# Optimization experiments

Measured on AMD Instinct MI355X. Metric: run time of the kernel, lower is better.

Reference implementation:

```python
import jax, jax.numpy as jnp
import numpy as np

B, S, H = 1, 2048, 4096
NQ, NKV, HD = 32, 8, 128
BLOCK = 128            # block size of block_streaming_attn_func
SINK_BLOCKS = 1        # sink_size 128 / BLOCK
LOCAL_BLOCKS = 8       # local_window_size 1024 / BLOCK
ROPE_BASE = 10000.0


def setup_inputs() -> dict:
    key = jax.random.key(0)
    ks = jax.random.split(key, 5)
    s = 0.02
    return {
        "hidden_states": jax.random.normal(ks[0], (B, S, H), jnp.float32),
        "wq": jax.random.normal(ks[1], (H, NQ * HD), jnp.float32) * s,
        "wk": jax.random.normal(ks[2], (H, NKV * HD), jnp.float32) * s,
        "wv": jax.random.normal(ks[3], (H, NKV * HD), jnp.float32) * s,
        "wo": jax.random.normal(ks[4], (NQ * HD, H), jnp.float32) * s,
    }


def _rope(x):
    # x: [B, S, heads, HD]; non-interleaved (GPT-NeoX half-split) rotary, full head_dim
    pos = jnp.arange(S, dtype=jnp.float32)
    inv = 1.0 / (ROPE_BASE ** (jnp.arange(0, HD, 2, dtype=jnp.float32) / HD))
    f = pos[:, None] * inv[None, :]                 # [S, HD/2]
    cos = jnp.cos(f)[None, :, None, :]
    sin = jnp.sin(f)[None, :, None, :]
    x1, x2 = x[..., : HD // 2], x[..., HD // 2 :]
    return jnp.concatenate([x1 * cos - x2 * sin, x2 * cos + x1 * sin], axis=-1).astype(x.dtype)


def _streaming_mask():
    # causal + (sink blocks OR local window blocks), block granularity = BLOCK
    idx = jnp.arange(S)
    blk = idx // BLOCK
    causal = idx[None, :] <= idx[:, None]
    sink = blk[None, :] < SINK_BLOCKS
    local = (blk[:, None] - blk[None, :]) < LOCAL_BLOCKS
    return causal & (sink | local)                  # [S, S]


def reference(hidden_states, wq, wk, wv, wo):
    q = (hidden_states @ wq).reshape(B, S, NQ, HD)
    k = (hidden_states @ wk).reshape(B, S, NKV, HD)
    v = (hidden_states @ wv).reshape(B, S, NKV, HD)
    q = _rope(q)
    k = _rope(k)
    rep = NQ // NKV                                 # repeat_kv (GQA)
    k = jnp.repeat(k, rep, axis=2)
    v = jnp.repeat(v, rep, axis=2)
    scores = jnp.einsum('bqhd,bkhd->bhqk', q, k) / jnp.sqrt(jnp.float32(HD))
    mask = _streaming_mask()
    scores = jnp.where(mask[None, None], scores, jnp.finfo(scores.dtype).min)
    p = jax.nn.softmax(scores, axis=-1)
    out = jnp.einsum('bhqk,bkhd->bqhd', p, v).reshape(B, S, NQ * HD)
    return out @ wo
```

## Files before the change

### kernel.cpp

```cpp
#include <hip/hip_runtime.h>
#include <hip/hip_bf16.h>
#include <math.h>

typedef __bf16 bf16;
typedef __attribute__((ext_vector_type(8))) __bf16 bf16x8;
typedef __attribute__((ext_vector_type(4))) __bf16 bf16x4;
typedef __attribute__((ext_vector_type(4))) float f32x4;

#define MFMA16(a, b, c) __builtin_amdgcn_mfma_f32_16x16x32_bf16(a, b, c, 0, 0, 0)

__device__ __forceinline__ void load16_lds(const bf16* g, bf16* l) {
  __builtin_amdgcn_global_load_lds(
      (const __attribute__((address_space(1))) void*)g,
      (__attribute__((address_space(3))) void*)l, 16, 0, 0);
}

__global__ __launch_bounds__(256) void cast_k(const float* __restrict__ src,
                                              bf16* __restrict__ dst) {
  const size_t i = ((size_t)blockIdx.x * 256 + threadIdx.x) * 8;
  f32x4 a = *(const f32x4*)(src + i);
  f32x4 b = *(const f32x4*)(src + i + 4);
  bf16x8 h;
#pragma unroll
  for (int j = 0; j < 4; ++j) {
    h[j] = (bf16)a[j];
    h[4 + j] = (bf16)b[j];
  }
  *(bf16x8*)(dst + i) = h;
}

__global__ __launch_bounds__(256) void transpose_cast_k(
    const float* __restrict__ src, bf16* __restrict__ dst, int rows,
    int cols) {
  __shared__ float tile[64][65];
  const int c0 = blockIdx.x * 64, r0 = blockIdx.y * 64;
  const int tid = threadIdx.x;
  const int lr = tid >> 4;
  const int lc = (tid & 15) * 4;
#pragma unroll
  for (int i = 0; i < 4; ++i) {
    const int row = lr + i * 16;
    const f32x4 v = *(const f32x4*)&src[(size_t)(r0 + row) * cols + c0 + lc];
#pragma unroll
    for (int j = 0; j < 4; ++j) tile[row][lc + j] = v[j];
  }
  __syncthreads();
#pragma unroll
  for (int i = 0; i < 4; ++i) {
    const int orow = lr + i * 16;
    bf16x4 h;
#pragma unroll
    for (int j = 0; j < 4; ++j) h[j] = (bf16)tile[lc + j][orow];
    *(bf16x4*)&dst[(size_t)(c0 + orow) * rows + r0 + lc] = h;
  }
}

template <typename OT, int EPI>
__global__ __launch_bounds__(256, 2) void gemm_bt(const bf16* __restrict__ A,
                                                  const bf16* __restrict__ Bt,
                                                  OT* __restrict__ C,
                                                  bf16* __restrict__ Ck,
                                                  bf16* __restrict__ C2, int M,
                                                  int N, int K, int ldc) {
  __shared__ bf16 As[128 * 32];
  __shared__ bf16 Bs[128 * 32];

  const int tid = threadIdx.x;
  const int lane = tid & 63;
  const int w = tid >> 6;
  const int quad = lane >> 4;
  const int m16 = lane & 15;
  const int wr = (w >> 1) * 64;
  const int wc = (w & 1) * 64;
  const int rowBase = blockIdx.y * 128;
  const int colBase = blockIdx.x * 128;

  f32x4 acc[4][4];
#pragma unroll
  for (int i = 0; i < 4; ++i)
#pragma unroll
    for (int j = 0; j < 4; ++j) acc[i][j] = (f32x4){0.f, 0.f, 0.f, 0.f};

  const int u1 = w * 128 + lane;
  const int u2 = u1 + 64;
  const int r1 = u1 >> 2, s1 = (u1 & 3) * 8;
  const int r2 = u2 >> 2, s2 = (u2 & 3) * 8;
  const bf16* aG1 = A + (size_t)(rowBase + r1) * K + s1;
  const bf16* aG2 = A + (size_t)(rowBase + r2) * K + s2;
  const bf16* bG1 = Bt + (size_t)(colBase + r1) * K + s1;
  const bf16* bG2 = Bt + (size_t)(colBase + r2) * K + s2;
  bf16* const lA1 = As + (size_t)(w * 128) * 8;
  bf16* const lA2 = As + (size_t)(w * 128 + 64) * 8;
  bf16* const lB1 = Bs + (size_t)(w * 128) * 8;
  bf16* const lB2 = Bs + (size_t)(w * 128 + 64) * 8;

  for (int k0 = 0; k0 < K; k0 += 32) {
    load16_lds(aG1 + k0, lA1);
    load16_lds(aG2 + k0, lA2);
    load16_lds(bG1 + k0, lB1);
    load16_lds(bG2 + k0, lB2);
    __syncthreads();

    bf16x8 af[4], bfr[4];
#pragma unroll
    for (int mi = 0; mi < 4; ++mi)
      af[mi] = *(const bf16x8*)&As[(wr + mi * 16 + m16) * 32 + quad * 8];
#pragma unroll
    for (int ni = 0; ni < 4; ++ni)
      bfr[ni] = *(const bf16x8*)&Bs[(wc + ni * 16 + m16) * 32 + quad * 8];
#pragma unroll
    for (int mi = 0; mi < 4; ++mi)
#pragma unroll
      for (int ni = 0; ni < 4; ++ni)
        acc[mi][ni] = MFMA16(af[mi], bfr[ni], acc[mi][ni]);
    __syncthreads();
  }

#pragma unroll
  for (int mi = 0; mi < 4; ++mi) {
#pragma unroll
    for (int ni = 0; ni < 4; ++ni) {
      const int gr0 = rowBase + wr + mi * 16 + quad * 4;
      const int gc = colBase + wc + ni * 16 + m16;
      if constexpr (EPI == 0) {
#pragma unroll
        for (int r = 0; r < 4; ++r)
          C[(size_t)(gr0 + r) * ldc + gc] = (OT)acc[mi][ni][r];
      } else {
        if (colBase < 4096) {
#pragma unroll
          for (int r = 0; r < 4; ++r)
            C[(size_t)(gr0 + r) * 4096 + gc] = (OT)acc[mi][ni][r];
        } else if (colBase < 5120) {
#pragma unroll
          for (int r = 0; r < 4; ++r)
            Ck[(size_t)(gr0 + r) * 1024 + (gc - 4096)] = (bf16)acc[mi][ni][r];
        } else {
          bf16x4 h;
#pragma unroll
          for (int r = 0; r < 4; ++r) h[r] = (bf16)acc[mi][ni][r];
          *(bf16x4*)&C2[(size_t)(gc - 5120) * 2048 + gr0] = h;
        }
      }
    }
  }
}

__global__ __launch_bounds__(256) void rope_k(bf16* __restrict__ qb,
                                              bf16* __restrict__ kb) {
  const int NQTOT = 2048 * 32 * 64;
  const int NKTOT = 2048 * 8 * 64;
  int idx = blockIdx.x * 256 + threadIdx.x;
  bf16* buf;
  int nh, rest;
  if (idx < NQTOT) {
    buf = qb;
    nh = 32;
    rest = idx;
  } else {
    rest = idx - NQTOT;
    if (rest >= NKTOT) return;
    buf = kb;
    nh = 8;
  }
  const int j = rest & 63;
  const int hs = rest >> 6;
  const int hh = hs % nh;
  const int s = hs / nh;
  const float inv = powf(10000.0f, -(float)j * (1.0f / 64.0f));
  const float f = (float)s * inv;
  float sn, cs;
  sincosf(f, &sn, &cs);
  const size_t base = (size_t)(s * nh + hh) * 128 + j;
  const float x1 = (float)buf[base];
  const float x2 = (float)buf[base + 64];
  buf[base] = (bf16)(x1 * cs - x2 * sn);
  buf[base + 64] = (bf16)(x2 * cs + x1 * sn);
}

__global__ __launch_bounds__(256, 2) void attn_k(const bf16* __restrict__ q,
                                                 const bf16* __restrict__ kbuf,
                                                 const bf16* __restrict__ vT,
                                                 bf16* __restrict__ attn) {
  const int qb = 15 - blockIdx.x;
  const int h = blockIdx.y;
  const int kvh = h >> 2;
  const int tid = threadIdx.x;
  const int lane = tid & 63;
  const int w = tid >> 6;
  const int quad = lane >> 4;
  const int m16 = lane & 15;

  __shared__ bf16 Ks[4][64 * 32];
  __shared__ bf16 Vs[2][128 * 32];
  __shared__ bf16 Ps[128][72];

  const int qrow0 = qb * 128 + w * 32;

  bf16x8 qf[2][4];
#pragma unroll
  for (int rt = 0; rt < 2; ++rt)
#pragma unroll
    for (int kt = 0; kt < 4; ++kt)
      qf[rt][kt] = *(const bf16x8*)&q[(size_t)(qrow0 + rt * 16 + m16) * 4096 +
                                      h * 128 + kt * 32 + quad * 8];

  f32x4 o[2][8];
  float lsum[2][4];
#pragma unroll
  for (int rt = 0; rt < 2; ++rt) {
#pragma unroll
    for (int dt = 0; dt < 8; ++dt) o[rt][dt] = (f32x4){0.f, 0.f, 0.f, 0.f};
#pragma unroll
    for (int r = 0; r < 4; ++r) lsum[rt][r] = 0.f;
  }

  const float scale = 0.08838834764831845f;
  const bf16* kbase = kbuf + kvh * 128;
  const bf16* vbase = vT + (size_t)(kvh * 128) * 2048;

  const int klocal = (lane >> 2);
  const int kseg = (lane & 3) * 8;

  for (int b = 0; b <= qb; ++b) {
    if (b > 0 && (qb - b) >= 8) continue;
    const bool diag = (b == qb);
    for (int half = 0; half < 2; ++half) {
      const int gk0 = b * 128 + half * 64;

#pragma unroll
      for (int i = 0; i < 4; ++i) {
        const int j = w * 4 + i;
        const int kt = j >> 2, grp = (j & 3) * 16;
        load16_lds(kbase + (size_t)(gk0 + grp + klocal) * 1024 + kt * 32 + kseg,
                   &Ks[kt][grp * 32]);
      }
#pragma unroll
      for (int i = 0; i < 4; ++i) {
        const int j = w * 4 + i;
        const int kc = j >> 3, grp = (j & 7) * 16;
        load16_lds(vbase + (size_t)(grp + klocal) * 2048 + gk0 + kc * 32 + kseg,
                   &Vs[kc][grp * 32]);
      }
      __syncthreads();

      const bool skip = diag && (half * 64 > w * 32 + 31);
      if (!skip) {
        f32x4 sc[2][4];
#pragma unroll
        for (int rt = 0; rt < 2; ++rt)
#pragma unroll
          for (int ct = 0; ct < 4; ++ct)
            sc[rt][ct] = (f32x4){0.f, 0.f, 0.f, 0.f};
#pragma unroll
        for (int kt = 0; kt < 4; ++kt) {
          bf16x8 kf[4];
#pragma unroll
          for (int ct = 0; ct < 4; ++ct)
            kf[ct] = *(const bf16x8*)&Ks[kt][(ct * 16 + m16) * 32 + quad * 8];
#pragma unroll
          for (int rt = 0; rt < 2; ++rt)
#pragma unroll
            for (int ct = 0; ct < 4; ++ct)
              sc[rt][ct] = MFMA16(qf[rt][kt], kf[ct], sc[rt][ct]);
        }

#pragma unroll
        for (int rt = 0; rt < 2; ++rt)
#pragma unroll
          for (int ct = 0; ct < 4; ++ct)
#pragma unroll
            for (int r = 0; r < 4; ++r) {
              float p = __expf(sc[rt][ct][r] * scale);
              if (diag) {
                const int colg = gk0 + ct * 16 + m16;
                const int rowg = qrow0 + rt * 16 + quad * 4 + r;
                if (colg > rowg) p = 0.f;
              }
              lsum[rt][r] += p;
              Ps[w * 32 + rt * 16 + quad * 4 + r][ct * 16 + m16] = (bf16)p;
            }

#pragma unroll
        for (int rt = 0; rt < 2; ++rt)
#pragma unroll
          for (int kc = 0; kc < 2; ++kc) {
            const bf16x8 pa =
                *(const bf16x8*)&Ps[w * 32 + rt * 16 + m16][kc * 32 + quad * 8];
#pragma unroll
            for (int dt = 0; dt < 8; ++dt) {
              const bf16x8 vb =
                  *(const bf16x8*)&Vs[kc][(dt * 16 + m16) * 32 + quad * 8];
              o[rt][dt] = MFMA16(pa, vb, o[rt][dt]);
            }
          }
      }
      __syncthreads();
    }
  }

#pragma unroll
  for (int rt = 0; rt < 2; ++rt) {
    float inv[4];
#pragma unroll
    for (int r = 0; r < 4; ++r) {
      float s = lsum[rt][r];
      s += __shfl_xor(s, 1);
      s += __shfl_xor(s, 2);
      s += __shfl_xor(s, 4);
      s += __shfl_xor(s, 8);
      inv[r] = 1.0f / s;
    }
#pragma unroll
    for (int dt = 0; dt < 8; ++dt)
#pragma unroll
      for (int r = 0; r < 4; ++r)
        attn[(size_t)(qrow0 + rt * 16 + quad * 4 + r) * 4096 + h * 128 +
             dt * 16 + m16] = (bf16)(o[rt][dt][r] * inv[r]);
  }
}

extern "C" void kernel_launch(void* const* d_in, const int* in_sizes, int n_in,
                              void* d_out, int out_size, void* d_ws,
                              size_t ws_size, hipStream_t stream) {
  const float* hidden = (const float*)d_in[0];
  const float* wq = (const float*)d_in[1];
  const float* wk = (const float*)d_in[2];
  const float* wv = (const float*)d_in[3];
  const float* wo = (const float*)d_in[4];
  float* out = (float*)d_out;

  const size_t MB = 1024 * 1024;
  bf16* hiddenB = (bf16*)d_ws;
  bf16* wqkvT = (bf16*)((char*)d_ws + 16 * MB);
  bf16* woT = (bf16*)d_ws;
  bf16* attnb = (bf16*)((char*)d_ws + 32 * MB);
  bf16* qbuf = (bf16*)((char*)d_ws + 64 * MB);
  bf16* kbuf = (bf16*)((char*)d_ws + 80 * MB);
  bf16* vT = (bf16*)((char*)d_ws + 84 * MB);

  cast_k<<<4096, 256, 0, stream>>>(hidden, hiddenB);
  transpose_cast_k<<<dim3(64, 64), 256, 0, stream>>>(wq, wqkvT, 4096, 4096);
  transpose_cast_k<<<dim3(16, 64), 256, 0, stream>>>(
      wk, wqkvT + (size_t)4096 * 4096, 4096, 1024);
  transpose_cast_k<<<dim3(16, 64), 256, 0, stream>>>(
      wv, wqkvT + (size_t)5120 * 4096, 4096, 1024);

  gemm_bt<bf16, 2><<<dim3(48, 16), 256, 0, stream>>>(
      hiddenB, wqkvT, qbuf, kbuf, vT, 2048, 6144, 4096, 4096);

  rope_k<<<(2048 * 32 * 64 + 2048 * 8 * 64) / 256, 256, 0, stream>>>(qbuf,
                                                                     kbuf);

  transpose_cast_k<<<dim3(64, 64), 256, 0, stream>>>(wo, woT, 4096, 4096);

  attn_k<<<dim3(16, 32), 256, 0, stream>>>(qbuf, kbuf, vT, attnb);

  gemm_bt<float, 0><<<dim3(32, 16), 256, 0, stream>>>(
      attnb, woT, out, nullptr, nullptr, 2048, 4096, 4096, 4096);
}
```

Baseline: 488.2 us.

## Replace QKV GEMM with 256x256-tile double-buffered 8-wave kernel; fast-math RoPE

Adds a dedicated QKV projection GEMM using 256x256 output tiles, 512 threads and 64-wide K steps. It double-buffers LDS with async global-to-LDS loads, uses an XOR-swizzled layout, and runs a barrier-interleaved schedule that alternates MFMA bursts (raised priority) with LDS reads and prefetches. The aim is more data reuse per tile and better overlap of loads with math than the old 128x128 generic kernel. The trade-off is a grid of only 192 blocks on a 256-CU part and heavy LDS use per block. RoPE also switches to __expf and __sincosf, which lose accuracy for large position angles.

```diff
diff --git a/kernel.cpp b/kernel.cpp
--- a/kernel.cpp
+++ b/kernel.cpp
@@ -52,6 +52,193 @@
 #pragma unroll
     for (int j = 0; j < 4; ++j) h[j] = (bf16)tile[lc + j][orow];
     *(bf16x4*)&dst[(size_t)(c0 + orow) * rows + r0 + lc] = h;
+  }
+}
+
+#define BARX() __builtin_amdgcn_s_barrier()
+#define SBAR0() __builtin_amdgcn_sched_barrier(0)
+#define LGKM0()                                       \
+  {                                                   \
+    asm volatile("s_waitcnt lgkmcnt(0)" ::: "memory");\
+    SBAR0();                                          \
+  }
+#define VMC(N)                                          \
+  {                                                     \
+    asm volatile("s_waitcnt vmcnt(" #N ")" ::: "memory");\
+    SBAR0();                                            \
+  }
+
+#define DS_A(BUF, QM)                                                       \
+  {                                                                         \
+    _Pragma("unroll") for (int mi = 0; mi < 4; ++mi)                        \
+        _Pragma("unroll") for (int kk = 0; kk < 2; ++kk)                    \
+            a[mi][kk] = *(const bf16x8*)&As[BUF][(aBase ^ (kk << 5)) +      \
+                                                (QM)*4096 + mi * 1024];     \
+  }
+
+#define DS_B(BUF, QN, BR)                                                   \
+  {                                                                         \
+    _Pragma("unroll") for (int ni = 0; ni < 2; ++ni)                        \
+        _Pragma("unroll") for (int kk = 0; kk < 2; ++kk)                    \
+            BR[ni][kk] = *(const bf16x8*)&Bs[BUF][(bBase ^ (kk << 5)) +     \
+                                                  (QN)*2048 + ni * 1024];   \
+  }
+
+#define MMAC(QM, QN, BR)                                                    \
+  {                                                                         \
+    __builtin_amdgcn_s_setprio(1);                                          \
+    _Pragma("unroll") for (int mi = 0; mi < 4; ++mi)                        \
+        _Pragma("unroll") for (int ni = 0; ni < 2; ++ni) {                  \
+      acc[(QM)*4 + mi][(QN)*2 + ni] =                                       \
+          MFMA16(a[mi][0], BR[ni][0], acc[(QM)*4 + mi][(QN)*2 + ni]);       \
+      acc[(QM)*4 + mi][(QN)*2 + ni] =                                       \
+          MFMA16(a[mi][1], BR[ni][1], acc[(QM)*4 + mi][(QN)*2 + ni]);       \
+    }                                                                       \
+    __builtin_amdgcn_s_setprio(0);                                          \
+  }
+
+#define STAGE_A(BUF, T)                                                     \
+  {                                                                         \
+    const bf16* g0 = aS0 + (size_t)(T)*64;                                  \
+    const bf16* g1 = aS1 + (size_t)(T)*64;                                  \
+    bf16* l = &As[BUF][w * 512];                                            \
+    load16_lds(g0, l);                                                      \
+    load16_lds(g1, l + 4096);                                               \
+    load16_lds(g0 + ROWK128, l + 8192);                                     \
+    load16_lds(g1 + ROWK128, l + 12288);                                    \
+  }
+
+#define STAGE_B(BUF, T)                                                     \
+  {                                                                         \
+    const bf16* g0 = bS0 + (size_t)(T)*64;                                  \
+    const bf16* g1 = bS1 + (size_t)(T)*64;                                  \
+    bf16* l = &Bs[BUF][w * 512];                                            \
+    load16_lds(g0, l);                                                      \
+    load16_lds(g1, l + 4096);                                               \
+    load16_lds(g0 + ROWK128, l + 8192);                                     \
+    load16_lds(g1 + ROWK128, l + 12288);                                    \
+  }
+
+__global__ __launch_bounds__(512, 2) void gemm_qkv256(
+    const bf16* __restrict__ A, const bf16* __restrict__ Bt,
+    bf16* __restrict__ Cq, bf16* __restrict__ Ck, bf16* __restrict__ Cv) {
+  constexpr int K = 4096;
+  constexpr size_t ROWK128 = (size_t)128 * K;
+  __shared__ bf16 As[2][256 * 64];
+  __shared__ bf16 Bs[2][256 * 64];
+
+  const int tid = threadIdx.x;
+  const int lane = tid & 63;
+  const int w = tid >> 6;
+  const int wm = w >> 2;
+  const int wn = w & 3;
+  const int quad = lane >> 4;
+  const int m16 = lane & 15;
+
+  const int rowBase = blockIdx.y * 256;
+  const int colBase = blockIdx.x * 256;
+
+  const int u0 = tid, u1 = 512 + tid;
+  const int r0 = u0 >> 3, c0s = (u0 & 7) ^ (r0 & 7);
+  const int r1 = u1 >> 3, c1s = (u1 & 7) ^ (r1 & 7);
+  const bf16* aS0 = A + (size_t)(rowBase + r0) * K + c0s * 8;
+  const bf16* aS1 = A + (size_t)(rowBase + r1) * K + c1s * 8;
+  const bf16* bS0 = Bt + (size_t)(colBase + r0) * K + c0s * 8;
+  const bf16* bS1 = Bt + (size_t)(colBase + r1) * K + c1s * 8;
+
+  const int xsw = (m16 & 7) << 3;
+  const int ko0 = (quad * 8) ^ xsw;
+  const int aBase = (wm * 128 + m16) * 64 + ko0;
+  const int bBase = (wn * 64 + m16) * 64 + ko0;
+
+  f32x4 acc[8][4];
+#pragma unroll
+  for (int i = 0; i < 8; ++i)
+#pragma unroll
+    for (int j = 0; j < 4; ++j) acc[i][j] = (f32x4){0.f, 0.f, 0.f, 0.f};
+
+  bf16x8 a[4][2], b0[2][2], b1[2][2];
+
+  STAGE_A(0, 0);
+  STAGE_B(0, 0);
+  STAGE_A(1, 1);
+  STAGE_B(1, 1);
+  VMC(8);
+  BARX();
+
+  constexpr int nT = K / 64;
+#pragma unroll 1
+  for (int i = 0; i < nT / 2; ++i) {
+    const int p0 = (2 * i + 2 < nT) ? 2 * i + 2 : 0;
+    const int p1 = (2 * i + 3 < nT) ? 2 * i + 3 : 0;
+    DS_A(0, 0);
+    DS_B(0, 0, b0);
+    BARX();
+    LGKM0();
+    MMAC(0, 0, b0);
+    BARX();
+    DS_B(0, 1, b1);
+    BARX();
+    LGKM0();
+    MMAC(0, 1, b1);
+    BARX();
+    DS_A(0, 1);
+    STAGE_B(0, p0);
+    BARX();
+    LGKM0();
+    MMAC(1, 0, b0);
+    BARX();
+    STAGE_A(0, p0);
+    VMC(6);
+    BARX();
+    MMAC(1, 1, b1);
+    BARX();
+    DS_A(1, 0);
+    DS_B(1, 0, b0);
+    BARX();
+    LGKM0();
+    MMAC(0, 0, b0);
+    BARX();
+    DS_B(1, 1, b1);
+    BARX();
+    LGKM0();
+    MMAC(0, 1, b1);
+    BARX();
+    DS_A(1, 1);
+    STAGE_B(1, p1);
+    BARX();
+    LGKM0();
+    MMAC(1, 0, b0);
+    BARX();
+    STAGE_A(1, p1);
+    VMC(6);
+    BARX();
+    MMAC(1, 1, b1);
+    BARX();
+  }
+  VMC(0);
+
+#pragma unroll
+  for (int am = 0; am < 8; ++am) {
+    const int gr0 = rowBase + wm * 128 + am * 16 + quad * 4;
+#pragma unroll
+    for (int an = 0; an < 4; ++an) {
+      const int gc = colBase + wn * 64 + an * 16 + m16;
+      if (colBase < 4096) {
+#pragma unroll
+        for (int r = 0; r < 4; ++r)
+          Cq[(size_t)(gr0 + r) * 4096 + gc] = (bf16)acc[am][an][r];
+      } else if (colBase < 5120) {
+#pragma unroll
+        for (int r = 0; r < 4; ++r)
+          Ck[(size_t)(gr0 + r) * 1024 + (gc - 4096)] = (bf16)acc[am][an][r];
+      } else {
+        bf16x4 h;
+#pragma unroll
+        for (int r = 0; r < 4; ++r) h[r] = (bf16)acc[am][an][r];
+        *(bf16x4*)&Cv[(size_t)(gc - 5120) * 2048 + gr0] = h;
+      }
+    }
   }
 }
 
@@ -126,21 +313,6 @@
 #pragma unroll
         for (int r = 0; r < 4; ++r)
           C[(size_t)(gr0 + r) * ldc + gc] = (OT)acc[mi][ni][r];
-      } else {
-        if (colBase < 4096) {
-#pragma unroll
-          for (int r = 0; r < 4; ++r)
-            C[(size_t)(gr0 + r) * 4096 + gc] = (OT)acc[mi][ni][r];
-        } else if (colBase < 5120) {
-#pragma unroll
-          for (int r = 0; r < 4; ++r)
-            Ck[(size_t)(gr0 + r) * 1024 + (gc - 4096)] = (bf16)acc[mi][ni][r];
-        } else {
-          bf16x4 h;
-#pragma unroll
-          for (int r = 0; r < 4; ++r) h[r] = (bf16)acc[mi][ni][r];
-          *(bf16x4*)&C2[(size_t)(gc - 5120) * 2048 + gr0] = h;
-        }
       }
     }
   }
@@ -167,10 +339,10 @@
   const int hs = rest >> 6;
   const int hh = hs % nh;
   const int s = hs / nh;
-  const float inv = powf(10000.0f, -(float)j * (1.0f / 64.0f));
+  const float inv = __expf((float)j * -0.14391157f);
   const float f = (float)s * inv;
   float sn, cs;
-  sincosf(f, &sn, &cs);
+  __sincosf(f, &sn, &cs);
   const size_t base = (size_t)(s * nh + hh) * 128 + j;
   const float x1 = (float)buf[base];
   const float x2 = (float)buf[base + 64];
@@ -346,8 +518,7 @@
   transpose_cast_k<<<dim3(16, 64), 256, 0, stream>>>(
       wv, wqkvT + (size_t)5120 * 4096, 4096, 1024);
 
-  gemm_bt<bf16, 2><<<dim3(48, 16), 256, 0, stream>>>(
-      hiddenB, wqkvT, qbuf, kbuf, vT, 2048, 6144, 4096, 4096);
+  gemm_qkv256<<<dim3(24, 8), 512, 0, stream>>>(hiddenB, wqkvT, qbuf, kbuf, vT);
 
   rope_k<<<(2048 * 32 * 64 + 2048 * 8 * 64) / 256, 256, 0, stream>>>(qbuf,
                                                                      kbuf);
```

After: 476.1 us. 2.5% less time.
